# Kernel tuning notes

Measured on AMD Instinct MI355X. Metric: run time of the kernel, lower is better.

## Reference

```python
import jax, jax.numpy as jnp
import numpy as np

B, D_IN, NQ, D_OUT = 65536, 1024, 64, 1024
PI = float(np.pi)


def setup_inputs() -> dict:
    key = jax.random.key(0)
    ks = jax.random.split(key, 6)
    return {
        "x": jax.random.normal(ks[0], (B, D_IN), dtype=jnp.float32),
        "W_in": jax.random.normal(ks[1], (NQ, D_IN), dtype=jnp.float32) * 0.02,
        "b_in": jax.random.normal(ks[2], (NQ,), dtype=jnp.float32) * 0.02,
        "quantum_params": jax.random.normal(ks[3], (NQ, 3), dtype=jnp.float32) * 0.1,
        "W_out": jax.random.normal(ks[4], (D_OUT, NQ), dtype=jnp.float32) * 0.02,
        "b_out": jax.random.normal(ks[5], (D_OUT,), dtype=jnp.float32) * 0.02,
    }


def reference(x, W_in, b_in, quantum_params, W_out, b_out):
    # input linear + tanh: [B, NQ]
    h = jnp.tanh(x @ W_in.T + b_in)
    # quantum forward, vectorized over (batch, qubit):
    # state = cos(h*pi/2)*cos(p0) + sin(p1)*cos(p2)
    angles = h * PI
    p0, p1, p2 = quantum_params[:, 0], quantum_params[:, 1], quantum_params[:, 2]
    state = jnp.cos(angles * 0.5) * jnp.cos(p0) + jnp.sin(p1) * jnp.cos(p2)
    # output linear: [B, D_OUT]
    return state @ W_out.T + b_out
```

## Files before the change

### kernel.cpp

```cpp
#include <hip/hip_runtime.h>
#include <hip/hip_bf16.h>
#include <math.h>

#define NB 65536
#define DIN 1024
#define NQ 64
#define DOUT 1024

typedef __attribute__((ext_vector_type(8))) short bf16x8;
typedef __attribute__((ext_vector_type(4))) float f32x4;
typedef unsigned short u16;

__device__ __forceinline__ u16 f2bf(float f) {
    union { float f; unsigned u; } v; v.f = f;
    return (u16)((v.u + 0x7fffu + ((v.u >> 16) & 1u)) >> 16);
}

__device__ __forceinline__ void gll16(const void* gsrc, void* ldst) {
    __builtin_amdgcn_global_load_lds(
        (const __attribute__((address_space(1))) unsigned int*)gsrc,
        (__attribute__((address_space(3))) unsigned int*)ldst, 16, 0, 0);
}

__global__ __launch_bounds__(256) void kP(const float* __restrict__ W_in,
                                          const float* __restrict__ W_out,
                                          const float* __restrict__ qp,
                                          u16* __restrict__ Wbf,
                                          u16* __restrict__ Wobf,
                                          float* __restrict__ cp0,
                                          float* __restrict__ cq) {
    int tid = blockIdx.x * 256 + threadIdx.x;
    {
        int j = tid & 7, l = (tid >> 3) & 63, n = (tid >> 9) & 3, c = tid >> 11;
        int row = n * 16 + (l & 15);
        int k   = c * 32 + (l >> 4) * 8 + j;
        Wbf[tid] = f2bf(W_in[row * DIN + k]);
    }
    {
        int j = tid & 7, l = (tid >> 3) & 63, kf = (tid >> 9) & 1, n = tid >> 10;
        int col = n * 16 + (l & 15);
        int k   = kf * 32 + (l >> 4) * 8 + j;
        Wobf[tid] = f2bf(W_out[col * NQ + k]);
    }
    if (tid < NQ) {
        cp0[tid] = cosf(qp[tid * 3 + 0]);
        cq[tid]  = sinf(qp[tid * 3 + 1]) * cosf(qp[tid * 3 + 2]);
    }
}

__global__ __launch_bounds__(256) void kF(const float* __restrict__ x,
                                          const u16* __restrict__ Wbf,
                                          const float* __restrict__ b_in,
                                          const float* __restrict__ cp0,
                                          const float* __restrict__ cq,
                                          const u16* __restrict__ Wobf,
                                          const float* __restrict__ b_out,
                                          float* __restrict__ out) {
    __shared__ __align__(16) char smem[24576];
    __shared__ u16 st[4][16][72];

    float* xs = (float*)smem;
    u16*  wbs = (u16*)(smem + 16384);

    const int tid = threadIdx.x;
    const int w = tid >> 6, l = tid & 63;
    const int r = l & 15, kg = l >> 4;
    const int row0 = blockIdx.x * 64;

    const int srow  = (w << 3) + (l >> 3);
    const int sslot = (l & 7) ^ (l >> 3);
    const float* xsrc0 = x + (size_t)(row0 + srow) * DIN + sslot * 4;
    const float* xsrc1 = xsrc0 + (size_t)32 * DIN;
    const int wl8 = (w * 64 + l) * 8;

    f32x4 acc[4] = {f32x4{0,0,0,0}, f32x4{0,0,0,0}, f32x4{0,0,0,0}, f32x4{0,0,0,0}};

    gll16(xsrc0, smem + (w << 10));
    gll16(xsrc1, smem + 4096 + (w << 10));
    gll16(Wbf + wl8, smem + 16384 + (w << 10));
    asm volatile("s_waitcnt vmcnt(0)" ::: "memory");
    __syncthreads();

    const int rowl = w * 16 + r;
    const int sw = r & 7;
    #pragma unroll 2
    for (int t = 0; t < 32; ++t) {
        const int cur = t & 1;
        if (t < 31) {
            const int nk = (t + 1) * 32;
            char* xb = smem + (cur ^ 1) * 8192;
            gll16(xsrc0 + nk, xb + (w << 10));
            gll16(xsrc1 + nk, xb + 4096 + (w << 10));
            gll16(Wbf + (size_t)(t + 1) * 2048 + wl8,
                  smem + 16384 + (cur ^ 1) * 4096 + (w << 10));
        } else {
            gll16(Wobf + wl8, smem + (w << 10));
            gll16(Wobf + 2048 + wl8, smem + 4096 + (w << 10));
        }
        const float* xr = xs + cur * 2048 + rowl * 32;
        float4 xa = *(const float4*)(xr + (((kg * 2) ^ sw) * 4));
        float4 xb = *(const float4*)(xr + (((kg * 2 + 1) ^ sw) * 4));
        union { bf16x8 v; unsigned u[4]; } a;
        asm("v_cvt_pk_bf16_f32 %0, %1, %2" : "=v"(a.u[0]) : "v"(xa.x), "v"(xa.y));
        asm("v_cvt_pk_bf16_f32 %0, %1, %2" : "=v"(a.u[1]) : "v"(xa.z), "v"(xa.w));
        asm("v_cvt_pk_bf16_f32 %0, %1, %2" : "=v"(a.u[2]) : "v"(xb.x), "v"(xb.y));
        asm("v_cvt_pk_bf16_f32 %0, %1, %2" : "=v"(a.u[3]) : "v"(xb.z), "v"(xb.w));
        const u16* wbuf = wbs + cur * 2048;
        #pragma unroll
        for (int n = 0; n < 4; ++n) {
            bf16x8 b = *(const bf16x8*)(wbuf + (n * 64 + l) * 8);
            acc[n] = __builtin_amdgcn_mfma_f32_16x16x32_bf16(a.v, b, acc[n], 0, 0, 0);
        }
        asm volatile("s_waitcnt vmcnt(0)" ::: "memory");
        __syncthreads();
    }

    #pragma unroll
    for (int n = 0; n < 4; ++n) {
        int q = n * 16 + r;
        float bi = b_in[q], c0q = cp0[q], c1q = cq[q];
        #pragma unroll
        for (int i = 0; i < 4; ++i) {
            float av = acc[n][i] + bi;
            float e2 = __builtin_amdgcn_exp2f(av * 2.8853900817779268f);
            float th = 1.0f - 2.0f * __builtin_amdgcn_rcpf(e2 + 1.0f);
            float s  = __builtin_amdgcn_cosf(th * 0.25f) * c0q + c1q;
            st[w][kg * 4 + i][q] = f2bf(s);
        }
    }
    __syncthreads();

    bf16x8 sa0 = *(const bf16x8*)&st[w][r][kg * 8];
    bf16x8 sa1 = *(const bf16x8*)&st[w][r][32 + kg * 8];
    const u16* wos = (const u16*)smem;
    const size_t orow = (size_t)(row0 + w * 16 + kg * 4) * DOUT;

    #pragma unroll 2
    for (int c = 0; c < 16; ++c) {
        const int cur = c & 1;
        if (c < 15) {
            char* ob = smem + (cur ^ 1) * 8192;
            const u16* src = Wobf + (size_t)(c + 1) * 4096 + wl8;
            gll16(src, ob + (w << 10));
            gll16(src + 2048, ob + 4096 + (w << 10));
        }
        const u16* buf = wos + cur * 4096;
        #pragma unroll
        for (int n = 0; n < 4; ++n) {
            bf16x8 b0 = *(const bf16x8*)(buf + ((n * 2 + 0) * 64 + l) * 8);
            bf16x8 b1 = *(const bf16x8*)(buf + ((n * 2 + 1) * 64 + l) * 8);
            f32x4 a2 = {0.0f, 0.0f, 0.0f, 0.0f};
            a2 = __builtin_amdgcn_mfma_f32_16x16x32_bf16(sa0, b0, a2, 0, 0, 0);
            a2 = __builtin_amdgcn_mfma_f32_16x16x32_bf16(sa1, b1, a2, 0, 0, 0);
            int col = (c * 4 + n) * 16 + r;
            float bo = b_out[col];
            #pragma unroll
            for (int i = 0; i < 4; ++i)
                out[orow + (size_t)i * DOUT + col] = a2[i] + bo;
        }
        asm volatile("s_waitcnt vmcnt(0)" ::: "memory");
        __syncthreads();
    }
}

extern "C" void kernel_launch(void* const* d_in, const int* in_sizes, int n_in,
                              void* d_out, int out_size, void* d_ws, size_t ws_size,
                              hipStream_t stream) {
    const float* x    = (const float*)d_in[0];
    const float* W_in = (const float*)d_in[1];
    const float* b_in = (const float*)d_in[2];
    const float* qp   = (const float*)d_in[3];
    const float* W_out= (const float*)d_in[4];
    const float* b_out= (const float*)d_in[5];
    float* out = (float*)d_out;

    char* ws = (char*)d_ws;
    u16*   Wbf  = (u16*)(ws);
    u16*   Wobf = (u16*)(ws + 131072);
    float* cp0  = (float*)(ws + 262144);
    float* cq   = (float*)(ws + 262400);

    kP<<<256, 256, 0, stream>>>(W_in, W_out, qp, Wbf, Wobf, cp0, cq);
    kF<<<NB / 64, 256, 0, stream>>>(x, Wbf, b_in, cp0, cq, Wobf, b_out, out);
}
```

Measured before the change: 162.7 us.

## Load operands directly into registers with a 3-deep prefetch pipeline and drop LDS staging

Both GEMM phases stop staging x, W_in and W_out tiles through LDS with global_load_lds and per-step __syncthreads. Each wave now loads its own fragments straight into registers with inline global_load_dwordx4, keeps them in a rotating 3-slot buffer, and uses partial vmcnt waits so that loads for step t+2 are in flight while step t computes. Biases and quantum constants are cached in LDS once, and the output is written with inline global stores. The aim is to remove block-wide barriers and LDS round-trips from a memory-bound streaming kernel. The cost is higher register pressure, repeated per-wave reads of the weights from cache instead of shared LDS copies, and vmcnt waits that also count the outstanding stores.

```diff
diff --git a/kernel.cpp b/kernel.cpp
--- a/kernel.cpp
+++ b/kernel.cpp
@@ -14,12 +14,6 @@
 __device__ __forceinline__ u16 f2bf(float f) {
     union { float f; unsigned u; } v; v.f = f;
     return (u16)((v.u + 0x7fffu + ((v.u >> 16) & 1u)) >> 16);
-}
-
-__device__ __forceinline__ void gll16(const void* gsrc, void* ldst) {
-    __builtin_amdgcn_global_load_lds(
-        (const __attribute__((address_space(1))) unsigned int*)gsrc,
-        (__attribute__((address_space(3))) unsigned int*)ldst, 16, 0, 0);
 }
 
 __global__ __launch_bounds__(256) void kP(const float* __restrict__ W_in,
@@ -56,111 +50,117 @@
                                           const u16* __restrict__ Wobf,
                                           const float* __restrict__ b_out,
                                           float* __restrict__ out) {
-    __shared__ __align__(16) char smem[24576];
-    __shared__ u16 st[4][16][72];
-
-    float* xs = (float*)smem;
-    u16*  wbs = (u16*)(smem + 16384);
+    __shared__ u16   st[4][16][72];
+    __shared__ float boutL[DOUT];
+    __shared__ float binL[NQ], cp0L[NQ], cqL[NQ];
 
     const int tid = threadIdx.x;
     const int w = tid >> 6, l = tid & 63;
     const int r = l & 15, kg = l >> 4;
     const int row0 = blockIdx.x * 64;
 
-    const int srow  = (w << 3) + (l >> 3);
-    const int sslot = (l & 7) ^ (l >> 3);
-    const float* xsrc0 = x + (size_t)(row0 + srow) * DIN + sslot * 4;
-    const float* xsrc1 = xsrc0 + (size_t)32 * DIN;
-    const int wl8 = (w * 64 + l) * 8;
+    *(float4*)(boutL + tid * 4) = *(const float4*)(b_out + tid * 4);
+    if (tid < NQ) { binL[tid] = b_in[tid]; cp0L[tid] = cp0[tid]; cqL[tid] = cq[tid]; }
+    __syncthreads();
+
+    const char* xS   = (const char*)x + (size_t)row0 * DIN * 4;
+    const char* outS = (const char*)out + (size_t)row0 * DOUT * 4;
+    const unsigned voff_x   = (unsigned)(w * 16 + r) * (DIN * 4) + kg * 32;
+    const unsigned voff_l16 = (unsigned)l * 16;
+    unsigned vo[4];
+    #pragma unroll
+    for (int i = 0; i < 4; i++)
+        vo[i] = (unsigned)(w * 16 + kg * 4 + i) * (DOUT * 4) + r * 4;
+
+#define LDX(slot, t) { \
+    asm volatile("global_load_dwordx4 %0, %1, %2 offset:%3" \
+        : "=v"(xr[slot][0]) : "v"(voff_x), "s"(xS), "i"((t) * 128)); \
+    asm volatile("global_load_dwordx4 %0, %1, %2 offset:%3" \
+        : "=v"(xr[slot][1]) : "v"(voff_x), "s"(xS), "i"((t) * 128 + 16)); }
+#define LDW(slot, t) { const char* wS_ = (const char*)Wbf + (t) * 4096; \
+    asm volatile("global_load_dwordx4 %0, %1, %2 offset:0"    : "=v"(wbr[slot][0]) : "v"(voff_l16), "s"(wS_)); \
+    asm volatile("global_load_dwordx4 %0, %1, %2 offset:1024" : "=v"(wbr[slot][1]) : "v"(voff_l16), "s"(wS_)); \
+    asm volatile("global_load_dwordx4 %0, %1, %2 offset:2048" : "=v"(wbr[slot][2]) : "v"(voff_l16), "s"(wS_)); \
+    asm volatile("global_load_dwordx4 %0, %1, %2 offset:3072" : "=v"(wbr[slot][3]) : "v"(voff_l16), "s"(wS_)); }
+#define PBLOAD(slot, g) { const char* oS_ = (const char*)Wobf + (g) * 4096; \
+    asm volatile("global_load_dwordx4 %0, %1, %2 offset:0"    : "=v"(wob[slot][0][0]) : "v"(voff_l16), "s"(oS_)); \
+    asm volatile("global_load_dwordx4 %0, %1, %2 offset:1024" : "=v"(wob[slot][0][1]) : "v"(voff_l16), "s"(oS_)); \
+    asm volatile("global_load_dwordx4 %0, %1, %2 offset:2048" : "=v"(wob[slot][1][0]) : "v"(voff_l16), "s"(oS_)); \
+    asm volatile("global_load_dwordx4 %0, %1, %2 offset:3072" : "=v"(wob[slot][1][1]) : "v"(voff_l16), "s"(oS_)); }
 
     f32x4 acc[4] = {f32x4{0,0,0,0}, f32x4{0,0,0,0}, f32x4{0,0,0,0}, f32x4{0,0,0,0}};
+    float4 xr[3][2];
+    bf16x8 wbr[3][4];
 
-    gll16(xsrc0, smem + (w << 10));
-    gll16(xsrc1, smem + 4096 + (w << 10));
-    gll16(Wbf + wl8, smem + 16384 + (w << 10));
-    asm volatile("s_waitcnt vmcnt(0)" ::: "memory");
-    __syncthreads();
+    LDX(0, 0) LDW(0, 0)
+    LDX(1, 1) LDW(1, 1)
 
-    const int rowl = w * 16 + r;
-    const int sw = r & 7;
-    #pragma unroll 2
+    #pragma unroll
     for (int t = 0; t < 32; ++t) {
-        const int cur = t & 1;
-        if (t < 31) {
-            const int nk = (t + 1) * 32;
-            char* xb = smem + (cur ^ 1) * 8192;
-            gll16(xsrc0 + nk, xb + (w << 10));
-            gll16(xsrc1 + nk, xb + 4096 + (w << 10));
-            gll16(Wbf + (size_t)(t + 1) * 2048 + wl8,
-                  smem + 16384 + (cur ^ 1) * 4096 + (w << 10));
-        } else {
-            gll16(Wobf + wl8, smem + (w << 10));
-            gll16(Wobf + 2048 + wl8, smem + 4096 + (w << 10));
-        }
-        const float* xr = xs + cur * 2048 + rowl * 32;
-        float4 xa = *(const float4*)(xr + (((kg * 2) ^ sw) * 4));
-        float4 xb = *(const float4*)(xr + (((kg * 2 + 1) ^ sw) * 4));
+        const int s = t % 3, s2 = (t + 2) % 3;
+        if (t + 2 < 32) { LDX(s2, t + 2) LDW(s2, t + 2) }
+        __builtin_amdgcn_sched_barrier(0);
+        if (t < 30)       asm volatile("s_waitcnt vmcnt(12)" ::: "memory");
+        else if (t == 30) asm volatile("s_waitcnt vmcnt(6)"  ::: "memory");
+        else              asm volatile("s_waitcnt vmcnt(0)"  ::: "memory");
+        __builtin_amdgcn_sched_barrier(0);
         union { bf16x8 v; unsigned u[4]; } a;
-        asm("v_cvt_pk_bf16_f32 %0, %1, %2" : "=v"(a.u[0]) : "v"(xa.x), "v"(xa.y));
-        asm("v_cvt_pk_bf16_f32 %0, %1, %2" : "=v"(a.u[1]) : "v"(xa.z), "v"(xa.w));
-        asm("v_cvt_pk_bf16_f32 %0, %1, %2" : "=v"(a.u[2]) : "v"(xb.x), "v"(xb.y));
-        asm("v_cvt_pk_bf16_f32 %0, %1, %2" : "=v"(a.u[3]) : "v"(xb.z), "v"(xb.w));
-        const u16* wbuf = wbs + cur * 2048;
+        asm("v_cvt_pk_bf16_f32 %0, %1, %2" : "=v"(a.u[0]) : "v"(xr[s][0].x), "v"(xr[s][0].y));
+        asm("v_cvt_pk_bf16_f32 %0, %1, %2" : "=v"(a.u[1]) : "v"(xr[s][0].z), "v"(xr[s][0].w));
+        asm("v_cvt_pk_bf16_f32 %0, %1, %2" : "=v"(a.u[2]) : "v"(xr[s][1].x), "v"(xr[s][1].y));
+        asm("v_cvt_pk_bf16_f32 %0, %1, %2" : "=v"(a.u[3]) : "v"(xr[s][1].z), "v"(xr[s][1].w));
         #pragma unroll
-        for (int n = 0; n < 4; ++n) {
-            bf16x8 b = *(const bf16x8*)(wbuf + (n * 64 + l) * 8);
-            acc[n] = __builtin_amdgcn_mfma_f32_16x16x32_bf16(a.v, b, acc[n], 0, 0, 0);
-        }
-        asm volatile("s_waitcnt vmcnt(0)" ::: "memory");
-        __syncthreads();
+        for (int n = 0; n < 4; ++n)
+            acc[n] = __builtin_amdgcn_mfma_f32_16x16x32_bf16(a.v, wbr[s][n], acc[n], 0, 0, 0);
     }
+
+    bf16x8 wob[3][2][2];
+    PBLOAD(0, 0) PBLOAD(1, 1)
+    __builtin_amdgcn_sched_barrier(0);
 
     #pragma unroll
     for (int n = 0; n < 4; ++n) {
         int q = n * 16 + r;
-        float bi = b_in[q], c0q = cp0[q], c1q = cq[q];
+        float bi = binL[q], c0q = cp0L[q], c1q = cqL[q];
         #pragma unroll
         for (int i = 0; i < 4; ++i) {
             float av = acc[n][i] + bi;
             float e2 = __builtin_amdgcn_exp2f(av * 2.8853900817779268f);
             float th = 1.0f - 2.0f * __builtin_amdgcn_rcpf(e2 + 1.0f);
-            float s  = __builtin_amdgcn_cosf(th * 0.25f) * c0q + c1q;
-            st[w][kg * 4 + i][q] = f2bf(s);
+            float sv = __builtin_amdgcn_cosf(th * 0.25f) * c0q + c1q;
+            st[w][kg * 4 + i][q] = f2bf(sv);
         }
     }
-    __syncthreads();
-
     bf16x8 sa0 = *(const bf16x8*)&st[w][r][kg * 8];
     bf16x8 sa1 = *(const bf16x8*)&st[w][r][32 + kg * 8];
-    const u16* wos = (const u16*)smem;
-    const size_t orow = (size_t)(row0 + w * 16 + kg * 4) * DOUT;
 
-    #pragma unroll 2
-    for (int c = 0; c < 16; ++c) {
-        const int cur = c & 1;
-        if (c < 15) {
-            char* ob = smem + (cur ^ 1) * 8192;
-            const u16* src = Wobf + (size_t)(c + 1) * 4096 + wl8;
-            gll16(src, ob + (w << 10));
-            gll16(src + 2048, ob + 4096 + (w << 10));
+    #pragma unroll
+    for (int g = 0; g < 32; ++g) {
+        const int s = g % 3, s2 = (g + 2) % 3;
+        if (g + 2 < 32) { PBLOAD(s2, g + 2) }
+        __builtin_amdgcn_sched_barrier(0);
+        if (g < 30)       asm volatile("s_waitcnt vmcnt(8)" ::: "memory");
+        else if (g == 30) asm volatile("s_waitcnt vmcnt(4)" ::: "memory");
+        else              asm volatile("s_waitcnt vmcnt(0)" ::: "memory");
+        __builtin_amdgcn_sched_barrier(0);
+        #pragma unroll
+        for (int ti = 0; ti < 2; ++ti) {
+            const int tile = g * 2 + ti;
+            f32x4 a2 = {0.0f, 0.0f, 0.0f, 0.0f};
+            a2 = __builtin_amdgcn_mfma_f32_16x16x32_bf16(sa0, wob[s][ti][0], a2, 0, 0, 0);
+            a2 = __builtin_amdgcn_mfma_f32_16x16x32_bf16(sa1, wob[s][ti][1], a2, 0, 0, 0);
+            float bo = boutL[tile * 16 + r];
+            #pragma unroll
+            for (int i = 0; i < 4; ++i) {
+                float d = a2[i] + bo;
+                asm volatile("global_store_dword %0, %1, %2 offset:%3"
+                             :: "v"(vo[i]), "v"(d), "s"(outS), "i"(tile * 64) : "memory");
+            }
         }
-        const u16* buf = wos + cur * 4096;
-        #pragma unroll
-        for (int n = 0; n < 4; ++n) {
-            bf16x8 b0 = *(const bf16x8*)(buf + ((n * 2 + 0) * 64 + l) * 8);
-            bf16x8 b1 = *(const bf16x8*)(buf + ((n * 2 + 1) * 64 + l) * 8);
-            f32x4 a2 = {0.0f, 0.0f, 0.0f, 0.0f};
-            a2 = __builtin_amdgcn_mfma_f32_16x16x32_bf16(sa0, b0, a2, 0, 0, 0);
-            a2 = __builtin_amdgcn_mfma_f32_16x16x32_bf16(sa1, b1, a2, 0, 0, 0);
-            int col = (c * 4 + n) * 16 + r;
-            float bo = b_out[col];
-            #pragma unroll
-            for (int i = 0; i < 4; ++i)
-                out[orow + (size_t)i * DOUT + col] = a2[i] + bo;
-        }
-        asm volatile("s_waitcnt vmcnt(0)" ::: "memory");
-        __syncthreads();
     }
+#undef LDX
+#undef LDW
+#undef PBLOAD
 }
 
 extern "C" void kernel_launch(void* const* d_in, const int* in_sizes, int n_in,
```

After: 165.0 us. Within noise of the previous version (+1.4%).
